# Optimization experiments

Hardware: AMD Instinct MI355X
Metric: run time of the kernel (lower is better)

Reference implementation:

```python
import jax, jax.numpy as jnp
from jax import lax
import numpy as np


def setup_inputs() -> dict:
    key = jax.random.key(0)
    kb, ks = jax.random.split(key)
    boxes = jax.random.uniform(kb, (4, 2048, 4), dtype=jnp.float32)
    scores = jax.random.normal(ks, (4, 16, 2048), dtype=jnp.float32)
    return {
        "boxes": boxes,
        "scores": scores,
        "max_output_boxes_per_class": 100,
        "iou_threshold": jnp.float32(0.5),
        "score_threshold": jnp.float32(0.0),
    }


def _fix_boxes(boxes):
    # center_point_box == 0 path: reorder corners so x1<=x2, y1<=y2
    # (swap-if-greater in the original is equivalent to per-axis min/max)
    x1, y1, x2, y2 = boxes[..., 0], boxes[..., 1], boxes[..., 2], boxes[..., 3]
    return jnp.stack(
        [jnp.minimum(x1, x2), jnp.minimum(y1, y2), jnp.maximum(x1, x2), jnp.maximum(y1, y2)],
        axis=-1,
    )


def _nms_single(boxes, scores, iou_thr, score_thr, K):
    # boxes: [N,4] (xyxy, already fixed), scores: [N]
    N = boxes.shape[0]
    order = jnp.argsort(-scores)  # stable sort -> ties broken by index, like torchvision
    b = boxes[order]
    x1, y1, x2, y2 = b[:, 0], b[:, 1], b[:, 2], b[:, 3]
    area = (x2 - x1) * (y2 - y1)
    idxs = jnp.arange(N)

    def step(suppressed, k):
        kept = ~suppressed[k]
        ix1 = jnp.maximum(b[k, 0], x1)
        iy1 = jnp.maximum(b[k, 1], y1)
        ix2 = jnp.minimum(b[k, 2], x2)
        iy2 = jnp.minimum(b[k, 3], y2)
        inter = jnp.maximum(ix2 - ix1, 0.0) * jnp.maximum(iy2 - iy1, 0.0)
        iou = inter / (area[k] + area - inter)
        suppressed = suppressed | (kept & (iou > iou_thr) & (idxs > k))
        return suppressed, kept

    _, keep = lax.scan(step, jnp.zeros((N,), bool), idxs)  # keep: [N] in score order
    rank = jnp.cumsum(keep) - 1
    slot = jnp.where(keep & (rank < K), rank, K)  # slot K is out-of-bounds -> dropped
    sel = jnp.full((K,), -1, jnp.int32).at[slot].set(order.astype(jnp.int32), mode="drop")
    # original truncates the top-K selection to the COUNT of selected boxes passing score_thr
    sel_valid = sel >= 0
    count = jnp.sum(sel_valid & (scores[jnp.maximum(sel, 0)] >= score_thr))
    return jnp.where(jnp.arange(K) < count, sel, -1)


def reference(boxes, scores, max_output_boxes_per_class, iou_threshold, score_threshold):
    B, N, _ = boxes.shape
    C = scores.shape[1]
    K = int(max_output_boxes_per_class)
    fb = _fix_boxes(boxes)
    f = lambda bx, sc: _nms_single(bx, sc, iou_threshold, score_threshold, K)
    # vmap over classes (boxes shared), then over batch
    sel = jax.vmap(jax.vmap(f, in_axes=(None, 0)), in_axes=(0, 0))(fb, scores)  # [B,C,K]
    valid = sel >= 0
    bidx = jnp.broadcast_to(jnp.arange(B, dtype=jnp.int32)[:, None, None], sel.shape)
    cidx = jnp.broadcast_to(jnp.arange(C, dtype=jnp.int32)[None, :, None], sel.shape)
    out = jnp.stack([jnp.where(valid, bidx, -1), jnp.where(valid, cidx, -1), sel], axis=-1)
    # fixed-shape padded version of the original ragged [num_selected, 3] output;
    # invalid rows are all -1
    return out.reshape(B * C * K, 3)
```

## Files before the change

### kernel.cpp

```cpp
#include <hip/hip_runtime.h>

#define NN 2048
#define NT 256
#define NB 4
#define NC 16
#define NCLS (NB * NC)
#define TILE 64
#define NTILES (NN / TILE)
#define KKEEP 176

typedef unsigned long long u64;

__device__ __forceinline__ unsigned score_hi(float s) {
  unsigned u = __float_as_uint(s);
  u ^= (u >> 31) ? 0xFFFFFFFFu : 0x80000000u;
  return ~u;
}
__device__ __forceinline__ float hi_score(unsigned hiw) {
  unsigned u = ~hiw;
  unsigned bits = (u >> 31) ? (u ^ 0x80000000u) : ~u;
  return __uint_as_float(bits);
}

__device__ __forceinline__ float iou_f(float kx1, float ky1, float kx2, float ky2, float ka,
                                       float x1, float y1, float x2, float y2, float a) {
  float ix1 = fmaxf(kx1, x1);
  float iy1 = fmaxf(ky1, y1);
  float ix2 = fminf(kx2, x2);
  float iy2 = fminf(ky2, y2);
  float iw = fmaxf(ix2 - ix1, 0.0f);
  float ih = fmaxf(iy2 - iy1, 0.0f);
  float inter = iw * ih;
  asm volatile("" : "+v"(inter));
  float denom = ka + a - inter;
  return inter / denom;
}

__global__ __launch_bounds__(NT) void rank_kernel(
    const float* __restrict__ scores,
    const float* __restrict__ boxes,
    float4* __restrict__ wbox,
    float* __restrict__ wsc, int* __restrict__ widx)
{
  __shared__ unsigned s_hi[NN];

  const int blk   = blockIdx.x;
  const int bc    = blk >> 3;
  const int chunk = blk & 7;
  const int b     = bc >> 4;
  const int t     = threadIdx.x;

  const float* __restrict__ scls = scores + (size_t)bc * NN;

  {
    const float4* s4 = (const float4*)scls;
    uint4* d4 = (uint4*)s_hi;
    float4 v = s4[t];
    d4[t] = make_uint4(score_hi(v.x), score_hi(v.y), score_hi(v.z), score_hi(v.w));
    v = s4[t + 256];
    d4[t + 256] = make_uint4(score_hi(v.x), score_hi(v.y), score_hi(v.z), score_hi(v.w));
  }
  __syncthreads();

  const int i0 = chunk * NT + t;
  const unsigned h0 = s_hi[i0];
  const u64 my0 = ((u64)h0 << 32) | (unsigned)i0;

  int c0 = 0, c1 = 0;
  const uint4* k4 = (const uint4*)s_hi;
#pragma unroll 2
  for (int jc = 0; jc < NN / 4; jc++) {
    const uint4 ka = k4[jc];
    const int j = jc * 4;
    u64 kj;
    kj = ((u64)ka.x << 32) | (unsigned)(j + 0); c0 += (kj < my0);
    kj = ((u64)ka.y << 32) | (unsigned)(j + 1); c1 += (kj < my0);
    kj = ((u64)ka.z << 32) | (unsigned)(j + 2); c0 += (kj < my0);
    kj = ((u64)ka.w << 32) | (unsigned)(j + 3); c1 += (kj < my0);
  }
  const int rank0 = c0 + c1;

  const float* __restrict__ bbase = boxes + (size_t)b * NN * 4;
  {
    float4 v = *(const float4*)(bbase + (size_t)i0 * 4);
    float x1 = fminf(v.x, v.z), x2 = fmaxf(v.x, v.z);
    float y1 = fminf(v.y, v.w), y2 = fmaxf(v.y, v.w);
    const size_t o = (size_t)bc * NN + rank0;
    wbox[o] = make_float4(x1, y1, x2, y2);
    wsc[o] = hi_score(h0); widx[o] = i0;
  }
}

__global__ __launch_bounds__(NT) void greedy_kernel(
    const float4* __restrict__ wbox,
    const float* __restrict__ wsc, const int* __restrict__ widx,
    const float* __restrict__ iou_thr_p, const float* __restrict__ score_thr_p,
    int K, int* __restrict__ out)
{
  __shared__ float4 s_tb[TILE];
  __shared__ float  s_ts[TILE];
  __shared__ int    s_tidx[TILE];
  __shared__ float4 s_kbox[KKEEP];
  __shared__ float  s_ka[KKEEP];
  __shared__ u64    s_colmask[4][TILE];
  __shared__ u64    s_dead[4];
  __shared__ int    s_total;

  const int bc = blockIdx.x;
  const int b  = bc >> 4;
  const int c  = bc & 15;
  const int t  = threadIdx.x;
  const int wv = t >> 6;
  const int ln = t & 63;

  const float iou_thr = *iou_thr_p;
  const float sthr    = *score_thr_p;

  int* orow = out + (size_t)bc * K * 3;
  for (int i = t; i < K * 3; i += NT) orow[i] = -1;
  if (t == 0) s_total = 0;

  const size_t base0 = (size_t)bc * NN;

  if      (wv == 1) s_tb[ln]   = wbox[base0 + ln];
  else if (wv == 2) s_ts[ln]   = wsc[base0 + ln];
  else if (wv == 3) s_tidx[ln] = widx[base0 + ln];
  __syncthreads();

  for (int tile = 0; tile < NTILES; tile++) {
    const float4 jb  = s_tb[ln];
    const float  jsc = s_ts[ln];
    const int    jidx = s_tidx[ln];
    const float  ja  = (jb.z - jb.x) * (jb.w - jb.y);
    const int kcount = s_total;

    const int pt = (tile + 1 < NTILES) ? tile + 1 : tile;
    float4 pb; float ps = 0.f; int pi = 0;
    if      (wv == 1) pb = wbox[base0 + pt * TILE + ln];
    else if (wv == 2) ps = wsc[base0 + pt * TILE + ln];
    else if (wv == 3) pi = widx[base0 + pt * TILE + ln];

    u64 m = 0ULL;
    for (int r = 0; r < 16; r++) {
      const int il = wv * 16 + r;
      if (il < ln) {
        const float4 rb = s_tb[il];
        const float ra = (rb.z - rb.x) * (rb.w - rb.y);
        const float iou = iou_f(rb.x, rb.y, rb.z, rb.w, ra,
                                jb.x, jb.y, jb.z, jb.w, ja);
        if (iou > iou_thr) m |= (1ULL << il);
      }
    }
    s_colmask[wv][ln] = m;

    bool dead = false;
    for (int ki = wv; ki < kcount; ki += 4) {
      const float4 kb = s_kbox[ki];
      const float iou = iou_f(kb.x, kb.y, kb.z, kb.w, s_ka[ki],
                              jb.x, jb.y, jb.z, jb.w, ja);
      if (iou > iou_thr) { dead = true; break; }
    }
    s_dead[wv] = __ballot(dead);
    __syncthreads();

    if (wv == 1)      s_tb[ln]   = pb;
    else if (wv == 2) s_ts[ln]   = ps;
    else if (wv == 3) s_tidx[ln] = pi;
    else {
      const u64 mc = s_colmask[0][ln] | s_colmask[1][ln] |
                     s_colmask[2][ln] | s_colmask[3][ln];
      u64 alive = ~(s_dead[0] | s_dead[1] | s_dead[2] | s_dead[3]);
      for (int i2 = 0; i2 < TILE; i2++) {
        if ((alive >> i2) & 1ULL) {
          const u64 kill = __ballot((int)((mc >> i2) & 1ULL));
          alive &= ~kill;
        }
      }
      const int total0 = s_total;
      const bool kept = (alive >> ln) & 1ULL;
      const int pos = __popcll(alive & ((1ULL << ln) - 1ULL));
      if (kept) {
        const int kpos = total0 + pos;
        s_kbox[kpos] = jb;
        s_ka[kpos]   = ja;
        if (kpos < K && jsc >= sthr) {
          orow[kpos * 3 + 0] = b;
          orow[kpos * 3 + 1] = c;
          orow[kpos * 3 + 2] = jidx;
        }
      }
      if (ln == 0) s_total = total0 + (int)__popcll(alive);
    }
    __syncthreads();
    if (s_total >= K) break;
  }
}

extern "C" void kernel_launch(void* const* d_in, const int* in_sizes, int n_in,
                              void* d_out, int out_size, void* d_ws, size_t ws_size,
                              hipStream_t stream) {
  const float* boxes  = (const float*)d_in[0];
  const float* scores = (const float*)d_in[1];
  const float* iou_p  = (const float*)d_in[3];
  const float* sth_p  = (const float*)d_in[4];
  int* out = (int*)d_out;

  const int K = out_size / (NCLS * 3);
  const size_t plane = (size_t)NCLS * NN;

  float4* wbox = (float4*)d_ws;
  float*  wsc  = (float*)(wbox + plane);
  int*    widx = (int*)(wsc + plane);

  hipLaunchKernelGGL(rank_kernel, dim3(NCLS * 8), dim3(NT), 0, stream,
                     scores, boxes, wbox, wsc, widx);
  hipLaunchKernelGGL(greedy_kernel, dim3(NCLS), dim3(NT), 0, stream,
                     wbox, wsc, widx, iou_p, sth_p, K, out);
}
```

Measured before the change: 60.87 us.

## Register-block rank counting and collapse greedy NMS to a single wavefront

```diff
diff --git a/kernel.cpp b/kernel.cpp
--- a/kernel.cpp
+++ b/kernel.cpp
@@ -36,6 +36,12 @@
   return inter / denom;
 }
 
+#define CMPK(HI, J, CC) do {                                   \
+  u64 kj = ((u64)(HI) << 32) | (unsigned)(J);                  \
+  CC[0] += (kj < my[0]); CC[1] += (kj < my[1]);                \
+  CC[2] += (kj < my[2]); CC[3] += (kj < my[3]);                \
+} while (0)
+
 __global__ __launch_bounds__(NT) void rank_kernel(
     const float* __restrict__ scores,
     const float* __restrict__ boxes,
@@ -43,12 +49,15 @@
     float* __restrict__ wsc, int* __restrict__ widx)
 {
   __shared__ unsigned s_hi[NN];
-
-  const int blk   = blockIdx.x;
-  const int bc    = blk >> 3;
-  const int chunk = blk & 7;
-  const int b     = bc >> 4;
-  const int t     = threadIdx.x;
+  __shared__ unsigned short s_part[4][4][64];
+
+  const int blk = blockIdx.x;
+  const int bc  = blk >> 3;
+  const int cb  = (blk & 7) * 256;
+  const int b   = bc >> 4;
+  const int t   = threadIdx.x;
+  const int wv  = t >> 6;
+  const int ln  = t & 63;
 
   const float* __restrict__ scls = scores + (size_t)bc * NN;
 
@@ -62,87 +71,95 @@
   }
   __syncthreads();
 
-  const int i0 = chunk * NT + t;
-  const unsigned h0 = s_hi[i0];
-  const u64 my0 = ((u64)h0 << 32) | (unsigned)i0;
-
-  int c0 = 0, c1 = 0;
+  u64 my[4];
+#pragma unroll
+  for (int i = 0; i < 4; i++) {
+    const int e = cb + ln + i * 64;
+    my[i] = ((u64)s_hi[e] << 32) | (unsigned)e;
+  }
+
+  int c0[4] = {0, 0, 0, 0}, c1[4] = {0, 0, 0, 0};
   const uint4* k4 = (const uint4*)s_hi;
+  const int kbase = wv * 128;
 #pragma unroll 2
-  for (int jc = 0; jc < NN / 4; jc++) {
-    const uint4 ka = k4[jc];
-    const int j = jc * 4;
-    u64 kj;
-    kj = ((u64)ka.x << 32) | (unsigned)(j + 0); c0 += (kj < my0);
-    kj = ((u64)ka.y << 32) | (unsigned)(j + 1); c1 += (kj < my0);
-    kj = ((u64)ka.z << 32) | (unsigned)(j + 2); c0 += (kj < my0);
-    kj = ((u64)ka.w << 32) | (unsigned)(j + 3); c1 += (kj < my0);
-  }
-  const int rank0 = c0 + c1;
-
-  const float* __restrict__ bbase = boxes + (size_t)b * NN * 4;
-  {
-    float4 v = *(const float4*)(bbase + (size_t)i0 * 4);
-    float x1 = fminf(v.x, v.z), x2 = fmaxf(v.x, v.z);
-    float y1 = fminf(v.y, v.w), y2 = fmaxf(v.y, v.w);
-    const size_t o = (size_t)bc * NN + rank0;
-    wbox[o] = make_float4(x1, y1, x2, y2);
-    wsc[o] = hi_score(h0); widx[o] = i0;
-  }
-}
-
-__global__ __launch_bounds__(NT) void greedy_kernel(
+  for (int jc = 0; jc < 64; jc++) {
+    const uint4 ka = k4[kbase + 2 * jc];
+    const uint4 kb = k4[kbase + 2 * jc + 1];
+    const int j = wv * 512 + jc * 8;
+    CMPK(ka.x, j + 0, c0); CMPK(ka.y, j + 1, c1);
+    CMPK(ka.z, j + 2, c0); CMPK(ka.w, j + 3, c1);
+    CMPK(kb.x, j + 4, c0); CMPK(kb.y, j + 5, c1);
+    CMPK(kb.z, j + 6, c0); CMPK(kb.w, j + 7, c1);
+  }
+#pragma unroll
+  for (int i = 0; i < 4; i++)
+    s_part[i][wv][ln] = (unsigned short)(c0[i] + c1[i]);
+  __syncthreads();
+
+  const int el = cb + ln + wv * 64;
+  const int rank = (int)s_part[wv][0][ln] + (int)s_part[wv][1][ln] +
+                   (int)s_part[wv][2][ln] + (int)s_part[wv][3][ln];
+  const unsigned h = s_hi[el];
+  float4 v = *(const float4*)(boxes + ((size_t)b * NN + el) * 4);
+  float x1 = fminf(v.x, v.z), x2 = fmaxf(v.x, v.z);
+  float y1 = fminf(v.y, v.w), y2 = fmaxf(v.y, v.w);
+  const size_t o = (size_t)bc * NN + rank;
+  wbox[o] = make_float4(x1, y1, x2, y2);
+  wsc[o]  = hi_score(h);
+  widx[o] = el;
+}
+
+__global__ __launch_bounds__(64) void greedy_kernel(
     const float4* __restrict__ wbox,
     const float* __restrict__ wsc, const int* __restrict__ widx,
     const float* __restrict__ iou_thr_p, const float* __restrict__ score_thr_p,
     int K, int* __restrict__ out)
 {
-  __shared__ float4 s_tb[TILE];
-  __shared__ float  s_ts[TILE];
-  __shared__ int    s_tidx[TILE];
   __shared__ float4 s_kbox[KKEEP];
   __shared__ float  s_ka[KKEEP];
-  __shared__ u64    s_colmask[4][TILE];
-  __shared__ u64    s_dead[4];
-  __shared__ int    s_total;
+  __shared__ float4 s_tb[TILE];
 
   const int bc = blockIdx.x;
   const int b  = bc >> 4;
   const int c  = bc & 15;
-  const int t  = threadIdx.x;
-  const int wv = t >> 6;
-  const int ln = t & 63;
+  const int ln = threadIdx.x;
 
   const float iou_thr = *iou_thr_p;
   const float sthr    = *score_thr_p;
 
   int* orow = out + (size_t)bc * K * 3;
-  for (int i = t; i < K * 3; i += NT) orow[i] = -1;
-  if (t == 0) s_total = 0;
+  for (int i = ln; i < K * 3; i += 64) orow[i] = -1;
 
   const size_t base0 = (size_t)bc * NN;
 
-  if      (wv == 1) s_tb[ln]   = wbox[base0 + ln];
-  else if (wv == 2) s_ts[ln]   = wsc[base0 + ln];
-  else if (wv == 3) s_tidx[ln] = widx[base0 + ln];
-  __syncthreads();
-
+  float4 jb  = wbox[base0 + ln];
+  float  jsc = wsc[base0 + ln];
+  int    jidx = widx[base0 + ln];
+
+  int total = 0;
   for (int tile = 0; tile < NTILES; tile++) {
-    const float4 jb  = s_tb[ln];
-    const float  jsc = s_ts[ln];
-    const int    jidx = s_tidx[ln];
-    const float  ja  = (jb.z - jb.x) * (jb.w - jb.y);
-    const int kcount = s_total;
-
-    const int pt = (tile + 1 < NTILES) ? tile + 1 : tile;
-    float4 pb; float ps = 0.f; int pi = 0;
-    if      (wv == 1) pb = wbox[base0 + pt * TILE + ln];
-    else if (wv == 2) ps = wsc[base0 + pt * TILE + ln];
-    else if (wv == 3) pi = widx[base0 + pt * TILE + ln];
+    s_tb[ln] = jb;
+    const float ja = (jb.z - jb.x) * (jb.w - jb.y);
+    const int kct = total;
+    __syncthreads();
+
+    float4 nb = jb; float ns = jsc; int ni = jidx;
+    if (tile + 1 < NTILES) {
+      nb = wbox[base0 + (tile + 1) * TILE + ln];
+      ns = wsc [base0 + (tile + 1) * TILE + ln];
+      ni = widx[base0 + (tile + 1) * TILE + ln];
+    }
+
+    bool dead = false;
+    for (int ki = 0; ki < kct; ki++) {
+      const float4 kb = s_kbox[ki];
+      const float iou = iou_f(kb.x, kb.y, kb.z, kb.w, s_ka[ki],
+                              jb.x, jb.y, jb.z, jb.w, ja);
+      if (iou > iou_thr) { dead = true; break; }
+    }
 
     u64 m = 0ULL;
-    for (int r = 0; r < 16; r++) {
-      const int il = wv * 16 + r;
+    for (int il = 0; il < TILE - 1; il++) {
       if (il < ln) {
         const float4 rb = s_tb[il];
         const float ra = (rb.z - rb.x) * (rb.w - rb.y);
@@ -151,48 +168,31 @@
         if (iou > iou_thr) m |= (1ULL << il);
       }
     }
-    s_colmask[wv][ln] = m;
-
-    bool dead = false;
-    for (int ki = wv; ki < kcount; ki += 4) {
-      const float4 kb = s_kbox[ki];
-      const float iou = iou_f(kb.x, kb.y, kb.z, kb.w, s_ka[ki],
-                              jb.x, jb.y, jb.z, jb.w, ja);
-      if (iou > iou_thr) { dead = true; break; }
-    }
-    s_dead[wv] = __ballot(dead);
+
+    u64 alive = __ballot(!dead);
+    for (int i2 = 0; i2 < TILE; i2++) {
+      if ((alive >> i2) & 1ULL) {
+        const u64 kill = __ballot((int)((m >> i2) & 1ULL));
+        alive &= ~kill;
+      }
+    }
+
+    const bool kept = (alive >> ln) & 1ULL;
+    const int pos = __popcll(alive & ((1ULL << ln) - 1ULL));
+    if (kept) {
+      const int kpos = total + pos;
+      s_kbox[kpos] = jb;
+      s_ka[kpos]   = ja;
+      if (kpos < K && jsc >= sthr) {
+        orow[kpos * 3 + 0] = b;
+        orow[kpos * 3 + 1] = c;
+        orow[kpos * 3 + 2] = jidx;
+      }
+    }
+    total += (int)__popcll(alive);
     __syncthreads();
-
-    if (wv == 1)      s_tb[ln]   = pb;
-    else if (wv == 2) s_ts[ln]   = ps;
-    else if (wv == 3) s_tidx[ln] = pi;
-    else {
-      const u64 mc = s_colmask[0][ln] | s_colmask[1][ln] |
-                     s_colmask[2][ln] | s_colmask[3][ln];
-      u64 alive = ~(s_dead[0] | s_dead[1] | s_dead[2] | s_dead[3]);
-      for (int i2 = 0; i2 < TILE; i2++) {
-        if ((alive >> i2) & 1ULL) {
-          const u64 kill = __ballot((int)((mc >> i2) & 1ULL));
-          alive &= ~kill;
-        }
-      }
-      const int total0 = s_total;
-      const bool kept = (alive >> ln) & 1ULL;
-      const int pos = __popcll(alive & ((1ULL << ln) - 1ULL));
-      if (kept) {
-        const int kpos = total0 + pos;
-        s_kbox[kpos] = jb;
-        s_ka[kpos]   = ja;
-        if (kpos < K && jsc >= sthr) {
-          orow[kpos * 3 + 0] = b;
-          orow[kpos * 3 + 1] = c;
-          orow[kpos * 3 + 2] = jidx;
-        }
-      }
-      if (ln == 0) s_total = total0 + (int)__popcll(alive);
-    }
-    __syncthreads();
-    if (s_total >= K) break;
+    if (total >= K) break;
+    jb = nb; jsc = ns; jidx = ni;
   }
 }
 
@@ -214,6 +214,6 @@
 
   hipLaunchKernelGGL(rank_kernel, dim3(NCLS * 8), dim3(NT), 0, stream,
                      scores, boxes, wbox, wsc, widx);
-  hipLaunchKernelGGL(greedy_kernel, dim3(NCLS), dim3(NT), 0, stream,
+  hipLaunchKernelGGL(greedy_kernel, dim3(NCLS), dim3(64), 0, stream,
                      wbox, wsc, widx, iou_p, sth_p, K, out);
 }
```

New measurement: 81.32 us. 1.34x slower.
